# Kernel tuning notes

Measured on AMD Instinct MI355X. Metric: run time of the kernel, lower is better.

The kernel has to match this reference:

```python
import jax, jax.numpy as jnp
import numpy as np

EPS = 1e-5


def setup_inputs() -> dict:
    key = jax.random.key(0)
    ks = jax.random.split(key, 24)
    B, S, D = 32, 1024, 768        # batch, num_segs, feature_dim
    E, G, C, P = 2, 8, 64, 384     # expansion, groups, num_clusters, latent_clus_dim
    EF = E * D                     # 1536
    GFS = EF // G                  # group_feature_size = 192
    s = 0.02
    f32 = jnp.float32
    return {
        "x": jax.random.normal(ks[0], (B, S, D), f32),
        "W_exp": s * jax.random.normal(ks[1], (D, EF), f32),
        "b_exp": jnp.zeros((EF,), f32),
        "W_ga": s * jax.random.normal(ks[2], (EF, G), f32),
        "b_ga": jnp.zeros((G,), f32),
        "bn1_g": jnp.ones((G * C,), f32) + 0.1 * jax.random.normal(ks[3], (G * C,), f32),
        "bn1_b": 0.1 * jax.random.normal(ks[4], (G * C,), f32),
        "bn1_m": 0.05 * jax.random.normal(ks[5], (G * C,), f32),
        "bn1_v": 1.0 + 0.1 * jax.random.uniform(ks[6], (G * C,), f32),
        "cluster_weights": s * jax.random.normal(ks[7], (EF, G * C), f32),
        "W_proj": s * jax.random.normal(ks[8], (GFS, D), f32),
        "b_proj": jnp.zeros((D,), f32),
        "bn2_g": jnp.ones((C,), f32) + 0.1 * jax.random.normal(ks[9], (C,), f32),
        "bn2_b": 0.1 * jax.random.normal(ks[10], (C,), f32),
        "bn2_m": 0.05 * jax.random.normal(ks[11], (C,), f32),
        "bn2_v": 1.0 + 0.1 * jax.random.uniform(ks[12], (C,), f32),
        "Wq": s * jax.random.normal(ks[13], (D, P), f32),
        "bq": jnp.zeros((P,), f32),
        "Wkv": s * jax.random.normal(ks[14], (D, 2 * P), f32),
        "bkv": jnp.zeros((2 * P,), f32),
        "Wp2": s * jax.random.normal(ks[15], (P, D), f32),
        "bp2": jnp.zeros((D,), f32),
    }


def reference(x, W_exp, b_exp, W_ga, b_ga, bn1_g, bn1_b, bn1_m, bn1_v,
              cluster_weights, W_proj, b_proj, bn2_g, bn2_b, bn2_m, bn2_v,
              Wq, bq, Wkv, bkv, Wp2, bp2):
    B, S, D = x.shape
    EF = W_exp.shape[1]
    G = W_ga.shape[1]
    C = bn2_g.shape[0]
    GFS = EF // G
    P = Wq.shape[1]

    fea = x @ W_exp + b_exp                                   # (B,S,EF)
    ga = jax.nn.sigmoid(fea @ W_ga + b_ga).reshape(B, S * G)  # (B,S*G)

    act = fea.reshape(B * S, EF) @ cluster_weights            # (B*S, G*C)
    act = (act - bn1_m) * (bn1_g / jnp.sqrt(bn1_v + EPS)) + bn1_b  # eval BN
    act = jax.nn.softmax(act.reshape(B, S * G, C), axis=-1) * ga[:, :, None]

    fea_g = fea.reshape(B, S * G, GFS)
    cent = jnp.einsum('bnc,bnf->bcf', act, fea_g)             # (B,C,GFS)

    nc = cent @ W_proj + b_proj                               # (B,C,D)
    scale2 = (bn2_g / jnp.sqrt(bn2_v + EPS))[None, :, None]
    nc = (nc - bn2_m[None, :, None]) * scale2 + bn2_b[None, :, None]

    q = x @ Wq + bq                                           # (B,S,P)
    kv = (nc @ Wkv + bkv).reshape(B, C, 2, P)
    k, v = kv[:, :, 0], kv[:, :, 1]

    scores = jnp.einsum('bsp,bcp->bsc', q, k) / jnp.sqrt(jnp.float32(P))
    attn = jax.nn.softmax(scores, axis=-1)                    # (B,S,C)
    out = jnp.einsum('bsc,bcp->bsp', attn, v)                 # (B,S,P)
    return out @ Wp2 + bp2                                    # (B,S,D)
```

## Files before the change

kernel.cpp:

```cpp
#include <hip/hip_runtime.h>
#include <hip/hip_bf16.h>

#define EPSV 1e-5f

namespace {
constexpr int Bn = 32, Sn = 1024, Dn = 768, Gn = 8, Cn = 64, Pn = 384;
constexpr int EFn = 1536, GFSn = 192, Nrows = Bn * Sn;
}

typedef __attribute__((ext_vector_type(8))) short short8;
typedef __attribute__((ext_vector_type(4))) float f32x4;
typedef __attribute__((ext_vector_type(16))) float f32x16;

__device__ __forceinline__ ushort f2bf(float f) {
  uint u = __builtin_bit_cast(uint, f);
  uint r = (u + 0x7fffu + ((u >> 16) & 1u)) >> 16;
  return (ushort)r;
}
__device__ __forceinline__ uint pack2bf(float lo, float hi) {
  return (uint)f2bf(lo) | ((uint)f2bf(hi) << 16);
}
__device__ __forceinline__ float bf2f(ushort h) {
  return __builtin_bit_cast(float, (uint)h << 16);
}
__device__ __forceinline__ void load16(const ushort* g, ushort* l) {
  __builtin_amdgcn_global_load_lds(
      (const __attribute__((address_space(1))) void*)g,
      (__attribute__((address_space(3))) void*)l, 16, 0, 0);
}
__device__ __forceinline__ int xcd_lid() {
  const int nbx = gridDim.x;
  const int nwg = nbx * gridDim.y;
  const int orig = blockIdx.y * nbx + blockIdx.x;
  const int xq = nwg >> 3, xr = nwg & 7;
  const int xcd = orig & 7, xi = orig >> 3;
  return (xcd < xr ? xcd * (xq + 1) : xr * (xq + 1) + (xcd - xr) * xq) + xi;
}

template <int MODE, int TRANS>
__global__ __launch_bounds__(256) void gemm_bf16(
    const ushort* __restrict__ A, const ushort* __restrict__ BT,
    const float* __restrict__ bias, void* __restrict__ Cout,
    ushort* __restrict__ Ct, int M, int N, int K,
    const float* __restrict__ g2, const float* __restrict__ b2,
    const float* __restrict__ m2, const float* __restrict__ v2,
    ushort* __restrict__ kq, ushort* __restrict__ vt) {
  __shared__ ushort sh[16384];
  const int tid = threadIdx.x;
  const int wave = tid >> 6, lane = tid & 63;
  const int nbx = gridDim.x;
  const int lid = xcd_lid();
  const int gm = (lid / nbx) * 128, gn = (lid % nbx) * 128;
  const int wr = wave >> 1, wc = wave & 1;

  const int sws = ((tid & 3) ^ ((tid >> 3) & 3)) * 8;
  const int c0 = tid, c1 = tid + 256;
  const ushort* gA0 = A + (size_t)(gm + (c0 >> 2)) * K + sws;
  const ushort* gA1 = A + (size_t)(gm + (c1 >> 2)) * K + sws;
  const ushort* gB0 = BT + (size_t)(gn + (c0 >> 2)) * K + sws;
  const ushort* gB1 = BT + (size_t)(gn + (c1 >> 2)) * K + sws;

  f32x4 acc[4][4] = {};
  const int l15 = lane & 15;
  const int arow = wr * 64 + l15;
  const int brow = wc * 64 + l15;
  const int kswz = (((lane >> 4) ^ ((l15 >> 1) & 3))) * 8;
  const int nk = K >> 5;

#define GB_STAGE(buf, k0)                                    \
  {                                                          \
    load16(gA0 + (k0), &sh[(buf)*8192 + wave * 512]);        \
    load16(gA1 + (k0), &sh[(buf)*8192 + 2048 + wave * 512]); \
    load16(gB0 + (k0), &sh[(buf)*8192 + 4096 + wave * 512]); \
    load16(gB1 + (k0), &sh[(buf)*8192 + 6144 + wave * 512]); \
  }

  GB_STAGE(0, 0);
  for (int t = 0; t < nk; ++t) {
    const int buf = t & 1;
    if (t + 1 < nk) {
      GB_STAGE(buf ^ 1, (t + 1) * 32);
      __builtin_amdgcn_sched_barrier(0);
      asm volatile("s_waitcnt vmcnt(4)" ::: "memory");
    } else {
      asm volatile("s_waitcnt vmcnt(0)" ::: "memory");
    }
    __builtin_amdgcn_s_barrier();
    __builtin_amdgcn_sched_barrier(0);
    short8 a[4], b[4];
#pragma unroll
    for (int m = 0; m < 4; ++m)
      a[m] = *reinterpret_cast<const short8*>(
          &sh[buf * 8192 + (arow + m * 16) * 32 + kswz]);
#pragma unroll
    for (int n = 0; n < 4; ++n)
      b[n] = *reinterpret_cast<const short8*>(
          &sh[buf * 8192 + 4096 + (brow + n * 16) * 32 + kswz]);
#pragma unroll
    for (int m = 0; m < 4; ++m)
#pragma unroll
      for (int n = 0; n < 4; ++n)
        acc[m][n] = __builtin_amdgcn_mfma_f32_16x16x32_bf16(
            a[m], b[n], acc[m][n], 0, 0, 0);
    __builtin_amdgcn_s_barrier();
    __builtin_amdgcn_sched_barrier(0);
  }
#undef GB_STAGE

  const int crow0 = gm + wr * 64 + (lane >> 4) * 4;
  const int ccol0 = gn + wc * 64 + l15;
  float sc_[4][4], sf_[4][4];
  if (MODE == 2) {
#pragma unroll
    for (int m = 0; m < 4; ++m)
#pragma unroll
      for (int j = 0; j < 4; ++j) {
        const int c = (crow0 + m * 16 + j) & 63;
        const float s = g2[c] * rsqrtf(v2[c] + EPSV);
        sc_[m][j] = s;
        sf_[m][j] = b2[c] - m2[c] * s;
      }
  }
  alignas(8) ushort cb[4][4][4];
#pragma unroll
  for (int m = 0; m < 4; ++m)
#pragma unroll
    for (int n = 0; n < 4; ++n) {
      const int col = ccol0 + n * 16;
      const float bv = bias ? bias[col] : 0.f;
#pragma unroll
      for (int j = 0; j < 4; ++j) {
        const int row = crow0 + m * 16 + j;
        float v = acc[m][n][j] + bv;
        if (MODE == 0) {
          ((float*)Cout)[(size_t)row * N + col] = v;
        } else if (MODE == 1) {
          const ushort h = f2bf(v);
          ((ushort*)Cout)[(size_t)row * N + col] = h;
          if (TRANS) cb[m][n][j] = h;
        } else if (MODE == 2) {
          v = v * sc_[m][j] + sf_[m][j];
          ((ushort*)Cout)[(size_t)row * N + col] = f2bf(v);
        } else {
          const ushort h = f2bf(v);
          if (col < 384) {
            kq[(size_t)row * 384 + col] = h;
          } else {
            vt[(size_t)(row >> 6) * 24576 + (size_t)(col - 384) * 64 +
               (row & 63)] = h;
          }
        }
      }
    }

  if (TRANS) {
    const int l4 = lane >> 4;
#pragma unroll
    for (int p = 0; p < 2; ++p) {
      __syncthreads();
      if (wc == p) {
#pragma unroll
        for (int n = 0; n < 4; ++n) {
          const int cl = n * 16 + l15;
#pragma unroll
          for (int m = 0; m < 4; ++m) {
            const int r = wr * 64 + m * 16 + l4 * 4;
            *reinterpret_cast<ushort4*>(&sh[cl * 136 + r]) =
                *reinterpret_cast<const ushort4*>(&cb[m][n][0]);
          }
        }
      }
      __syncthreads();
      const int cl = tid >> 2, seg = tid & 3;
      const ushort* src = &sh[cl * 136 + seg * 32];
      ushort* dst = Ct + (size_t)(gn + p * 64 + cl) * M + gm + seg * 32;
      *reinterpret_cast<uint4*>(dst) = *reinterpret_cast<const uint4*>(src);
      *reinterpret_cast<uint4*>(dst + 8) =
          *reinterpret_cast<const uint4*>(src + 8);
      *reinterpret_cast<uint4*>(dst + 16) =
          *reinterpret_cast<const uint4*>(src + 16);
      *reinterpret_cast<uint4*>(dst + 24) =
          *reinterpret_cast<const uint4*>(src + 24);
    }
  }
}

__global__ __launch_bounds__(256) void gemm_ga(
    const ushort* __restrict__ fea, const ushort* __restrict__ WTga,
    const float* __restrict__ b_ga, float* __restrict__ ga) {
  constexpr int K = EFn;
  __shared__ ushort sh[9216];
  const int tid = threadIdx.x;
  const int wave = tid >> 6, lane = tid & 63;
  const int gm = blockIdx.x * 128;

  const int sws = ((tid & 3) ^ ((tid >> 3) & 3)) * 8;
  const int swsB = ((lane & 3) ^ ((lane >> 3) & 3)) * 8;
  const int c0 = tid, c1 = tid + 256;
  const ushort* gA0 = fea + (size_t)(gm + (c0 >> 2)) * K + sws;
  const ushort* gA1 = fea + (size_t)(gm + (c1 >> 2)) * K + sws;
  const ushort* gB = WTga + (size_t)(lane >> 2) * K + swsB;

  f32x4 acc[2] = {};
  const int l15 = lane & 15, l4 = lane >> 4;
  const int kswz = ((l4 ^ ((l15 >> 1) & 3))) * 8;

#define GA_STAGE(buf, k0)                                     \
  {                                                           \
    load16(gA0 + (k0), &sh[(buf)*4608 + wave * 512]);         \
    load16(gA1 + (k0), &sh[(buf)*4608 + 2048 + wave * 512]);  \
    if (wave == 0) load16(gB + (k0), &sh[(buf)*4608 + 4096]); \
  }

  GA_STAGE(0, 0);
  for (int t = 0; t < K / 32; ++t) {
    const int buf = t & 1;
    if (t + 1 < K / 32) {
      GA_STAGE(buf ^ 1, (t + 1) * 32);
      __builtin_amdgcn_sched_barrier(0);
      asm volatile("s_waitcnt vmcnt(2)" ::: "memory");
    } else {
      asm volatile("s_waitcnt vmcnt(0)" ::: "memory");
    }
    __builtin_amdgcn_s_barrier();
    __builtin_amdgcn_sched_barrier(0);
    const short8 b = *reinterpret_cast<const short8*>(
        &sh[buf * 4608 + 4096 + l15 * 32 + kswz]);
    short8 a[2];
#pragma unroll
    for (int mi = 0; mi < 2; ++mi)
      a[mi] = *reinterpret_cast<const short8*>(
          &sh[buf * 4608 + (wave * 32 + mi * 16 + l15) * 32 + kswz]);
#pragma unroll
    for (int mi = 0; mi < 2; ++mi)
      acc[mi] =
          __builtin_amdgcn_mfma_f32_16x16x32_bf16(a[mi], b, acc[mi], 0, 0, 0);
    __builtin_amdgcn_s_barrier();
    __builtin_amdgcn_sched_barrier(0);
  }
#undef GA_STAGE

  if (l15 < 8) {
    const float bv = b_ga[l15];
#pragma unroll
    for (int mi = 0; mi < 2; ++mi)
#pragma unroll
      for (int j = 0; j < 4; ++j) {
        const int row = gm + wave * 32 + mi * 16 + l4 * 4 + j;
        const float v = acc[mi][j] + bv;
        ga[(size_t)row * 8 + l15] = 1.0f / (1.0f + expf(-v));
      }
  }
}

__global__ __launch_bounds__(256) void gemm_sm(
    const ushort* __restrict__ A, const ushort* __restrict__ BT,
    const float* __restrict__ g1, const float* __restrict__ b1,
    const float* __restrict__ m1, const float* __restrict__ v1,
    const float* __restrict__ ga, ushort* __restrict__ actT) {
  constexpr int K = EFn, N = Nrows;
  __shared__ ushort sh[16384];
  __shared__ float sScale[128], sShift[128];
  const int tid = threadIdx.x;
  const int wave = tid >> 6, lane = tid & 63;
  const int lid = xcd_lid();
  const int gm = (lid & 3) * 128;
  const int gn = (lid >> 2) * 128;
  const int wr = wave >> 1, wc = wave & 1;

  if (tid < 128) {
    const int row = gm + tid;
    const float sc = g1[row] * rsqrtf(v1[row] + EPSV);
    sScale[tid] = sc;
    sShift[tid] = b1[row] - m1[row] * sc;
  }

  const int sws = ((tid & 3) ^ ((tid >> 3) & 3)) * 8;
  const int c0 = tid, c1 = tid + 256;
  const ushort* gA0 = A + (size_t)(gm + (c0 >> 2)) * K + sws;
  const ushort* gA1 = A + (size_t)(gm + (c1 >> 2)) * K + sws;
  const ushort* gB0 = BT + (size_t)(gn + (c0 >> 2)) * K + sws;
  const ushort* gB1 = BT + (size_t)(gn + (c1 >> 2)) * K + sws;

  f32x4 acc[4][4] = {};
  const int l15 = lane & 15;
  const int arow = wr * 64 + l15;
  const int brow = wc * 64 + l15;
  const int kswz = (((lane >> 4) ^ ((l15 >> 1) & 3))) * 8;
  const int nk = K >> 5;

#define SM_STAGE(buf, k0)                                    \
  {                                                          \
    load16(gA0 + (k0), &sh[(buf)*8192 + wave * 512]);        \
    load16(gA1 + (k0), &sh[(buf)*8192 + 2048 + wave * 512]); \
    load16(gB0 + (k0), &sh[(buf)*8192 + 4096 + wave * 512]); \
    load16(gB1 + (k0), &sh[(buf)*8192 + 6144 + wave * 512]); \
  }

  SM_STAGE(0, 0);
  for (int t = 0; t < nk; ++t) {
    const int buf = t & 1;
    if (t + 1 < nk) {
      SM_STAGE(buf ^ 1, (t + 1) * 32);
      __builtin_amdgcn_sched_barrier(0);
      asm volatile("s_waitcnt vmcnt(4)" ::: "memory");
    } else {
      asm volatile("s_waitcnt vmcnt(0)" ::: "memory");
    }
    __builtin_amdgcn_s_barrier();
    __builtin_amdgcn_sched_barrier(0);
    short8 a[4], b[4];
#pragma unroll
    for (int m = 0; m < 4; ++m)
      a[m] = *reinterpret_cast<const short8*>(
          &sh[buf * 8192 + (arow + m * 16) * 32 + kswz]);
#pragma unroll
    for (int n = 0; n < 4; ++n)
      b[n] = *reinterpret_cast<const short8*>(
          &sh[buf * 8192 + 4096 + (brow + n * 16) * 32 + kswz]);
#pragma unroll
    for (int m = 0; m < 4; ++m)
#pragma unroll
      for (int n = 0; n < 4; ++n)
        acc[m][n] = __builtin_amdgcn_mfma_f32_16x16x32_bf16(
            a[m], b[n], acc[m][n], 0, 0, 0);
    __builtin_amdgcn_s_barrier();
    __builtin_amdgcn_sched_barrier(0);
  }
#undef SM_STAGE

  const int l4 = lane >> 4;
  const int g = (gm >> 6) + wr;
#pragma unroll
  for (int n = 0; n < 4; ++n) {
    const int col = gn + wc * 64 + n * 16 + l15;
    float mx = -1e30f;
#pragma unroll
    for (int m = 0; m < 4; ++m)
#pragma unroll
      for (int j = 0; j < 4; ++j) {
        const int rl = wr * 64 + m * 16 + l4 * 4 + j;
        acc[m][n][j] = acc[m][n][j] * sScale[rl] + sShift[rl];
        mx = fmaxf(mx, acc[m][n][j]);
      }
    mx = fmaxf(mx, __shfl_xor(mx, 16));
    mx = fmaxf(mx, __shfl_xor(mx, 32));
    float sum = 0.f;
#pragma unroll
    for (int m = 0; m < 4; ++m)
#pragma unroll
      for (int j = 0; j < 4; ++j) {
        acc[m][n][j] = expf(acc[m][n][j] - mx);
        sum += acc[m][n][j];
      }
    sum += __shfl_xor(sum, 16);
    sum += __shfl_xor(sum, 32);
    const float sc = ga[(size_t)col * 8 + g] / sum;
#pragma unroll
    for (int m = 0; m < 4; ++m)
#pragma unroll
      for (int j = 0; j < 4; ++j) {
        const int rowg = gm + wr * 64 + m * 16 + l4 * 4 + j;
        actT[(size_t)rowg * N + col] = f2bf(acc[m][n][j] * sc);
      }
  }
}

__global__ __launch_bounds__(256) void cvt_kernel(const float* __restrict__ in,
                                                  ushort* __restrict__ out,
                                                  int n4) {
  const int i = blockIdx.x * 256 + threadIdx.x;
  if (i >= n4) return;
  const float4 v = reinterpret_cast<const float4*>(in)[i];
  ushort4 o;
  o.x = f2bf(v.x); o.y = f2bf(v.y); o.z = f2bf(v.z); o.w = f2bf(v.w);
  reinterpret_cast<ushort4*>(out)[i] = o;
}

__global__ __launch_bounds__(256) void tconv_kernel(const float* __restrict__ in,
                                                    ushort* __restrict__ out,
                                                    int R, int C) {
  __shared__ float t[32][33];
  const int tx = threadIdx.x & 31, ty = threadIdx.x >> 5;
  const int bc = blockIdx.x * 32, br = blockIdx.y * 32;
#pragma unroll
  for (int i = 0; i < 32; i += 8)
    t[ty + i][tx] = in[(size_t)(br + ty + i) * C + bc + tx];
  __syncthreads();
#pragma unroll
  for (int i = 0; i < 32; i += 8)
    out[(size_t)(bc + ty + i) * R + br + tx] = f2bf(t[tx][ty + i]);
}

__global__ __launch_bounds__(256) void gawt_kernel(const float* __restrict__ in,
                                                   ushort* __restrict__ out) {
  const int k = blockIdx.x * 256 + threadIdx.x;
#pragma unroll
  for (int g = 0; g < 8; ++g) {
    out[(size_t)g * EFn + k] = f2bf(in[(size_t)k * 8 + g]);
    out[(size_t)(g + 8) * EFn + k] = 0;
  }
}

__global__ __launch_bounds__(256) void cent_mfma(
    const ushort* __restrict__ actT, const ushort* __restrict__ feaT,
    float* __restrict__ part) {
  __shared__ ushort As[2][64 * 64];
  __shared__ ushort Bs[2][192 * 64];
  const int tid = threadIdx.x;
  const int wave = tid >> 6, lane = tid & 63;
  const int b = blockIdx.x >> 4;
  const int g = (blockIdx.x >> 1) & 7;
  const int ch = blockIdx.x & 1;
  const size_t colbase = (size_t)b * 1024 + ch * 512;
  const int srow = tid >> 2, scp = (tid & 3) * 2;
  const ushort* gA = actT + (size_t)(g * 64 + srow) * Nrows + colbase;
  const ushort* gB0 = feaT + (size_t)(g * 192 + srow) * Nrows + colbase;
  const ushort* gB1 = gB0 + (size_t)64 * Nrows;
  const ushort* gB2 = gB0 + (size_t)128 * Nrows;

  uint4 ra[2], rb0[2], rb1[2], rb2[2];
  f32x4 acc[4][3] = {};
  const int l15 = lane & 15, hi = lane >> 4;
  const int sw = srow & 7;

#define CM_ISSUE(k0)                                                    \
  {                                                                     \
    _Pragma("unroll") for (int i = 0; i < 2; ++i) {                     \
      const int off = (k0) + (scp + i) * 8;                             \
      ra[i] = *reinterpret_cast<const uint4*>(gA + off);                \
      rb0[i] = *reinterpret_cast<const uint4*>(gB0 + off);              \
      rb1[i] = *reinterpret_cast<const uint4*>(gB1 + off);              \
      rb2[i] = *reinterpret_cast<const uint4*>(gB2 + off);              \
    }                                                                   \
  }
#define CM_STASH(buf)                                                   \
  {                                                                     \
    _Pragma("unroll") for (int i = 0; i < 2; ++i) {                     \
      const int c = scp + i;                                            \
      *reinterpret_cast<uint4*>(&As[buf][srow * 64 + ((c ^ sw) * 8)]) = \
          ra[i];                                                        \
      *reinterpret_cast<uint4*>(&Bs[buf][srow * 64 + ((c ^ sw) * 8)]) = \
          rb0[i];                                                       \
      *reinterpret_cast<uint4*>(                                        \
          &Bs[buf][(64 + srow) * 64 + ((c ^ sw) * 8)]) = rb1[i];        \
      *reinterpret_cast<uint4*>(                                        \
          &Bs[buf][(128 + srow) * 64 + ((c ^ sw) * 8)]) = rb2[i];       \
    }                                                                   \
  }

  CM_ISSUE(0);
  CM_STASH(0);
  for (int kk = 0; kk < 8; ++kk) {
    const int buf = kk & 1;
    __syncthreads();
    if (kk < 7) CM_ISSUE((kk + 1) * 64);
#pragma unroll
    for (int ks = 0; ks < 2; ++ks) {
      const int chh = ks * 4 + hi;
      short8 a[4], bb[3];
#pragma unroll
      for (int m = 0; m < 4; ++m) {
        const int r = m * 16 + l15;
        a[m] = *reinterpret_cast<const short8*>(
            &As[buf][r * 64 + ((chh ^ (r & 7)) * 8)]);
      }
#pragma unroll
      for (int nn = 0; nn < 3; ++nn) {
        const int r = wave * 48 + nn * 16 + l15;
        bb[nn] = *reinterpret_cast<const short8*>(
            &Bs[buf][r * 64 + ((chh ^ (r & 7)) * 8)]);
      }
#pragma unroll
      for (int m = 0; m < 4; ++m)
#pragma unroll
        for (int nn = 0; nn < 3; ++nn)
          acc[m][nn] = __builtin_amdgcn_mfma_f32_16x16x32_bf16(
              a[m], bb[nn], acc[m][nn], 0, 0, 0);
    }
    if (kk < 7) CM_STASH(buf ^ 1);
  }
#undef CM_ISSUE
#undef CM_STASH

  float* pb = part + (size_t)blockIdx.x * 12288;
#pragma unroll
  for (int m = 0; m < 4; ++m)
#pragma unroll
    for (int nn = 0; nn < 3; ++nn) {
      const int col = wave * 48 + nn * 16 + l15;
#pragma unroll
      for (int j = 0; j < 4; ++j) {
        const int row = m * 16 + hi * 4 + j;
        pb[row * 192 + col] = acc[m][nn][j];
      }
    }
}

__global__ __launch_bounds__(256) void cent_reduce8(
    const float* __restrict__ part, ushort* __restrict__ cent) {
  const int idx = blockIdx.x * 256 + threadIdx.x;
  const int b = idx / 12288, r = idx % 12288;
  float s = 0.f;
#pragma unroll
  for (int j = 0; j < 16; ++j) s += part[(size_t)(b * 16 + j) * 12288 + r];
  cent[idx] = f2bf(s);
}

__global__ __launch_bounds__(256) void attn_mfma(
    const ushort* __restrict__ qb, const ushort* __restrict__ kb,
    const ushort* __restrict__ vtb, ushort* __restrict__ aout) {
  const int wave = threadIdx.x >> 6, lane = threadIdx.x & 63;
  const int wrow = blockIdx.x * 4 + wave;
  const int row0 = wrow * 32;
  const int b = row0 >> 10;
  const int l31 = lane & 31, hi = lane >> 5;

  f32x16 accs0 = 0.f, accs1 = 0.f;
  const ushort* qp = qb + (size_t)(row0 + l31) * 384 + hi * 8;
  const ushort* kp = kb + (size_t)(b * 64 + l31) * 384 + hi * 8;
#pragma unroll 4
  for (int ks = 0; ks < 24; ++ks) {
    const short8 bq = *reinterpret_cast<const short8*>(qp + ks * 16);
    const short8 a0 = *reinterpret_cast<const short8*>(kp + ks * 16);
    const short8 a1 = *reinterpret_cast<const short8*>(kp + 32 * 384 + ks * 16);
    accs0 = __builtin_amdgcn_mfma_f32_32x32x16_bf16(a0, bq, accs0, 0, 0, 0);
    accs1 = __builtin_amdgcn_mfma_f32_32x32x16_bf16(a1, bq, accs1, 0, 0, 0);
  }

  const float alpha = 0.05103103630798287f;
  float p[32];
#pragma unroll
  for (int i = 0; i < 16; ++i) { p[i] = accs0[i]; p[16 + i] = accs1[i]; }
  float mx = p[0];
#pragma unroll
  for (int i = 1; i < 32; ++i) mx = fmaxf(mx, p[i]);
  mx = fmaxf(mx, __shfl_xor(mx, 32));
  float sum = 0.f;
#pragma unroll
  for (int i = 0; i < 32; ++i) {
    p[i] = expf((p[i] - mx) * alpha);
    sum += p[i];
  }
  sum += __shfl_xor(sum, 32);
  const float inv = 1.0f / sum;

  uint pk0[8], pk1[8];
#pragma unroll
  for (int ct = 0; ct < 2; ++ct)
#pragma unroll
    for (int rg = 0; rg < 4; ++rg) {
      pk0[ct * 4 + rg] =
          pack2bf(p[ct * 16 + rg * 4 + 0] * inv, p[ct * 16 + rg * 4 + 1] * inv);
      pk1[ct * 4 + rg] =
          pack2bf(p[ct * 16 + rg * 4 + 2] * inv, p[ct * 16 + rg * 4 + 3] * inv);
    }
  uint ex0[8], ex1[8];
#pragma unroll
  for (int i = 0; i < 8; ++i) {
    ex0[i] = __shfl_xor(pk0[i], 32);
    ex1[i] = __shfl_xor(pk1[i], 32);
  }

  const ushort* vp = vtb + ((size_t)b * 384 + l31) * 64 + hi * 8;
  ushort* orow = aout + (size_t)(row0 + l31) * 384;
  for (int mt = 0; mt < 12; ++mt) {
    f32x16 acco = 0.f;
#pragma unroll
    for (int kc = 0; kc < 4; ++kc) {
      const short8 av = *reinterpret_cast<const short8*>(
          vp + (size_t)mt * 32 * 64 + kc * 16);
      const int base = (kc >> 1) * 4 + (kc & 1) * 2;
      const uint o0 = hi ? pk0[base + 1] : pk0[base];
      const uint o1 = hi ? pk1[base + 1] : pk1[base];
      const uint e0 = hi ? ex0[base + 1] : ex0[base];
      const uint e1 = hi ? ex1[base + 1] : ex1[base];
      uint4 uu;
      uu.x = hi ? e0 : o0;
      uu.y = hi ? e1 : o1;
      uu.z = hi ? o0 : e0;
      uu.w = hi ? o1 : e1;
      const short8 bp = __builtin_bit_cast(short8, uu);
      acco = __builtin_amdgcn_mfma_f32_32x32x16_bf16(av, bp, acco, 0, 0, 0);
    }
#pragma unroll
    for (int rg = 0; rg < 4; ++rg) {
      ushort4 ov;
      ov.x = f2bf(acco[rg * 4 + 0]);
      ov.y = f2bf(acco[rg * 4 + 1]);
      ov.z = f2bf(acco[rg * 4 + 2]);
      ov.w = f2bf(acco[rg * 4 + 3]);
      *reinterpret_cast<ushort4*>(&orow[mt * 32 + rg * 8 + hi * 4]) = ov;
    }
  }
}

extern "C" void kernel_launch(void* const* d_in, const int* in_sizes, int n_in,
                              void* d_out, int out_size, void* d_ws,
                              size_t ws_size, hipStream_t stream) {
  (void)in_sizes; (void)n_in; (void)out_size; (void)ws_size;
  const float* x      = (const float*)d_in[0];
  const float* W_exp  = (const float*)d_in[1];
  const float* b_exp  = (const float*)d_in[2];
  const float* W_ga   = (const float*)d_in[3];
  const float* b_ga   = (const float*)d_in[4];
  const float* bn1_g  = (const float*)d_in[5];
  const float* bn1_b  = (const float*)d_in[6];
  const float* bn1_m  = (const float*)d_in[7];
  const float* bn1_v  = (const float*)d_in[8];
  const float* cw     = (const float*)d_in[9];
  const float* W_proj = (const float*)d_in[10];
  const float* b_proj = (const float*)d_in[11];
  const float* bn2_g  = (const float*)d_in[12];
  const float* bn2_b  = (const float*)d_in[13];
  const float* bn2_m  = (const float*)d_in[14];
  const float* bn2_v  = (const float*)d_in[15];
  const float* Wq     = (const float*)d_in[16];
  const float* bq     = (const float*)d_in[17];
  const float* Wkv    = (const float*)d_in[18];
  const float* bkv    = (const float*)d_in[19];
  const float* Wp2    = (const float*)d_in[20];
  const float* bp2    = (const float*)d_in[21];
  float* out = (float*)d_out;

  char* ws = (char*)d_ws;
  ushort* fea  = (ushort*)(ws + 0);
  ushort* aout = (ushort*)(ws + 0);
  ushort* xb   = (ushort*)(ws + 100663296ull);
  ushort* actT = (ushort*)(ws + 100663296ull);
  ushort* q_bf = (ushort*)(ws + 150994944ull);
  float*  ga   = (float*)(ws + 176160768ull);
  float*  part = (float*)(ws + 177209344ull);
  ushort* WT1  = (ushort*)(ws + 202375168ull);
  ushort* WT2  = (ushort*)(ws + 204734464ull);
  ushort* WT3  = (ushort*)(ws + 206307328ull);
  ushort* WT4  = (ushort*)(ws + 206897152ull);
  ushort* WT5  = (ushort*)(ws + 207486976ull);
  ushort* WT6  = (ushort*)(ws + 207781888ull);
  ushort* WTga = (ushort*)(ws + 208961536ull);
  ushort* cent = (ushort*)(ws + 209010688ull);
  ushort* nc   = (ushort*)(ws + 209797120ull);
  ushort* k_bf = (ushort*)(ws + 212942848ull);
  ushort* vT_bf= (ushort*)(ws + 214515712ull);
  ushort* feaT = (ushort*)d_out;

  dim3 blk(256);
  cvt_kernel<<<dim3((Nrows * Dn / 4 + 255) / 256), blk, 0, stream>>>(
      x, xb, Nrows * Dn / 4);
  tconv_kernel<<<dim3(EFn / 32, Dn / 32), blk, 0, stream>>>(W_exp, WT1, Dn, EFn);
  tconv_kernel<<<dim3(512 / 32, EFn / 32), blk, 0, stream>>>(cw, WT2, EFn, 512);
  tconv_kernel<<<dim3(Pn / 32, Dn / 32), blk, 0, stream>>>(Wq, WT3, Dn, Pn);
  tconv_kernel<<<dim3(Dn / 32, Pn / 32), blk, 0, stream>>>(Wp2, WT4, Pn, Dn);
  tconv_kernel<<<dim3(Dn / 32, GFSn / 32), blk, 0, stream>>>(W_proj, WT5, GFSn, Dn);
  tconv_kernel<<<dim3(Dn / 32, Dn / 32), blk, 0, stream>>>(Wkv, WT6, Dn, Dn);
  gawt_kernel<<<dim3(EFn / 256), blk, 0, stream>>>(W_ga, WTga);
  gemm_bf16<1, 1><<<dim3(EFn / 128, Nrows / 128), blk, 0, stream>>>(
      xb, WT1, b_exp, fea, feaT, Nrows, EFn, Dn,
      nullptr, nullptr, nullptr, nullptr, nullptr, nullptr);
  gemm_bf16<1, 0><<<dim3(Pn / 128, Nrows / 128), blk, 0, stream>>>(
      xb, WT3, bq, q_bf, nullptr, Nrows, Pn, Dn,
      nullptr, nullptr, nullptr, nullptr, nullptr, nullptr);
  gemm_ga<<<dim3(Nrows / 128), blk, 0, stream>>>(fea, WTga, b_ga, ga);
  gemm_sm<<<dim3(Nrows / 128, 512 / 128), blk, 0, stream>>>(
      WT2, fea, bn1_g, bn1_b, bn1_m, bn1_v, ga, actT);
  cent_mfma<<<dim3(Bn * Gn * 2), blk, 0, stream>>>(actT, feaT, part);
  cent_reduce8<<<dim3(393216 / 256), blk, 0, stream>>>(part, cent);
  gemm_bf16<2, 0><<<dim3(Dn / 128, 2048 / 128), blk, 0, stream>>>(
      cent, WT5, b_proj, nc, nullptr, 2048, Dn, GFSn,
      bn2_g, bn2_b, bn2_m, bn2_v, nullptr, nullptr);
  gemm_bf16<3, 0><<<dim3(Dn / 128, 2048 / 128), blk, 0, stream>>>(
      nc, WT6, bkv, nullptr, nullptr, 2048, Dn, Dn,
      nullptr, nullptr, nullptr, nullptr, k_bf, vT_bf);
  attn_mfma<<<dim3(Nrows / 128), blk, 0, stream>>>(q_bf, k_bf, vT_bf, aout);
  gemm_bf16<0, 0><<<dim3(Dn / 128, Nrows / 128), blk, 0, stream>>>(
      aout, WT4, bp2, out, nullptr, Nrows, Dn, Pn,
      nullptr, nullptr, nullptr, nullptr, nullptr, nullptr);
}
```

Baseline: 465.4 us.

## Triple-buffer GEMM pipelines and drop transposed fea copy in centroid kernel

Moves gemm_bf16, gemm_ga and gemm_sm from double to triple buffered LDS staging, prefetching two K-tiles ahead with adjusted waitcnts to hide more global latency. Also removes the transposed feaT output written by the expansion GEMM. cent_mfma now reads the row-major fea directly and transposes it in registers before storing to LDS. This cuts a large transposed global write and its LDS shuffle, at the cost of strided loads in cent_mfma and more LDS per block, which may lower occupancy.

```diff
diff --git a/kernel.cpp b/kernel.cpp
--- a/kernel.cpp
+++ b/kernel.cpp
@@ -37,15 +37,15 @@
   return (xcd < xr ? xcd * (xq + 1) : xr * (xq + 1) + (xcd - xr) * xq) + xi;
 }
 
-template <int MODE, int TRANS>
+template <int MODE>
 __global__ __launch_bounds__(256) void gemm_bf16(
     const ushort* __restrict__ A, const ushort* __restrict__ BT,
     const float* __restrict__ bias, void* __restrict__ Cout,
-    ushort* __restrict__ Ct, int M, int N, int K,
+    int M, int N, int K,
     const float* __restrict__ g2, const float* __restrict__ b2,
     const float* __restrict__ m2, const float* __restrict__ v2,
     ushort* __restrict__ kq, ushort* __restrict__ vt) {
-  __shared__ ushort sh[16384];
+  __shared__ ushort sh[24576];
   const int tid = threadIdx.x;
   const int wave = tid >> 6, lane = tid & 63;
   const int nbx = gridDim.x;
@@ -76,11 +76,15 @@
   }
 
   GB_STAGE(0, 0);
+  GB_STAGE(1, 32);
+  int bc = 0;
   for (int t = 0; t < nk; ++t) {
-    const int buf = t & 1;
-    if (t + 1 < nk) {
-      GB_STAGE(buf ^ 1, (t + 1) * 32);
+    if (t + 2 < nk) {
+      const int bp = (bc == 0) ? 2 : bc - 1;
+      GB_STAGE(bp, (t + 2) * 32);
       __builtin_amdgcn_sched_barrier(0);
+      asm volatile("s_waitcnt vmcnt(8)" ::: "memory");
+    } else if (t + 1 < nk) {
       asm volatile("s_waitcnt vmcnt(4)" ::: "memory");
     } else {
       asm volatile("s_waitcnt vmcnt(0)" ::: "memory");
@@ -91,11 +95,11 @@
 #pragma unroll
     for (int m = 0; m < 4; ++m)
       a[m] = *reinterpret_cast<const short8*>(
-          &sh[buf * 8192 + (arow + m * 16) * 32 + kswz]);
+          &sh[bc * 8192 + (arow + m * 16) * 32 + kswz]);
 #pragma unroll
     for (int n = 0; n < 4; ++n)
       b[n] = *reinterpret_cast<const short8*>(
-          &sh[buf * 8192 + 4096 + (brow + n * 16) * 32 + kswz]);
+          &sh[bc * 8192 + 4096 + (brow + n * 16) * 32 + kswz]);
 #pragma unroll
     for (int m = 0; m < 4; ++m)
 #pragma unroll
@@ -104,6 +108,7 @@
             a[m], b[n], acc[m][n], 0, 0, 0);
     __builtin_amdgcn_s_barrier();
     __builtin_amdgcn_sched_barrier(0);
+    bc = (bc == 2) ? 0 : bc + 1;
   }
 #undef GB_STAGE
 
@@ -121,7 +126,6 @@
         sf_[m][j] = b2[c] - m2[c] * s;
       }
   }
-  alignas(8) ushort cb[4][4][4];
 #pragma unroll
   for (int m = 0; m < 4; ++m)
 #pragma unroll
@@ -135,9 +139,7 @@
         if (MODE == 0) {
           ((float*)Cout)[(size_t)row * N + col] = v;
         } else if (MODE == 1) {
-          const ushort h = f2bf(v);
-          ((ushort*)Cout)[(size_t)row * N + col] = h;
-          if (TRANS) cb[m][n][j] = h;
+          ((ushort*)Cout)[(size_t)row * N + col] = f2bf(v);
         } else if (MODE == 2) {
           v = v * sc_[m][j] + sf_[m][j];
           ((ushort*)Cout)[(size_t)row * N + col] = f2bf(v);
@@ -152,44 +154,13 @@
         }
       }
     }
-
-  if (TRANS) {
-    const int l4 = lane >> 4;
-#pragma unroll
-    for (int p = 0; p < 2; ++p) {
-      __syncthreads();
-      if (wc == p) {
-#pragma unroll
-        for (int n = 0; n < 4; ++n) {
-          const int cl = n * 16 + l15;
-#pragma unroll
-          for (int m = 0; m < 4; ++m) {
-            const int r = wr * 64 + m * 16 + l4 * 4;
-            *reinterpret_cast<ushort4*>(&sh[cl * 136 + r]) =
-                *reinterpret_cast<const ushort4*>(&cb[m][n][0]);
-          }
-        }
-      }
-      __syncthreads();
-      const int cl = tid >> 2, seg = tid & 3;
-      const ushort* src = &sh[cl * 136 + seg * 32];
-      ushort* dst = Ct + (size_t)(gn + p * 64 + cl) * M + gm + seg * 32;
-      *reinterpret_cast<uint4*>(dst) = *reinterpret_cast<const uint4*>(src);
-      *reinterpret_cast<uint4*>(dst + 8) =
-          *reinterpret_cast<const uint4*>(src + 8);
-      *reinterpret_cast<uint4*>(dst + 16) =
-          *reinterpret_cast<const uint4*>(src + 16);
-      *reinterpret_cast<uint4*>(dst + 24) =
-          *reinterpret_cast<const uint4*>(src + 24);
-    }
-  }
 }
 
 __global__ __launch_bounds__(256) void gemm_ga(
     const ushort* __restrict__ fea, const ushort* __restrict__ WTga,
     const float* __restrict__ b_ga, float* __restrict__ ga) {
   constexpr int K = EFn;
-  __shared__ ushort sh[9216];
+  __shared__ ushort sh[13824];
   const int tid = threadIdx.x;
   const int wave = tid >> 6, lane = tid & 63;
   const int gm = blockIdx.x * 128;
@@ -204,6 +175,7 @@
   f32x4 acc[2] = {};
   const int l15 = lane & 15, l4 = lane >> 4;
   const int kswz = ((l4 ^ ((l15 >> 1) & 3))) * 8;
+  constexpr int nk = K / 32;
 
 #define GA_STAGE(buf, k0)                                     \
   {                                                           \
@@ -213,30 +185,41 @@
   }
 
   GA_STAGE(0, 0);
-  for (int t = 0; t < K / 32; ++t) {
-    const int buf = t & 1;
-    if (t + 1 < K / 32) {
-      GA_STAGE(buf ^ 1, (t + 1) * 32);
+  GA_STAGE(1, 32);
+  int bc = 0;
+  for (int t = 0; t < nk; ++t) {
+    if (t + 2 < nk) {
+      const int bp = (bc == 0) ? 2 : bc - 1;
+      GA_STAGE(bp, (t + 2) * 32);
       __builtin_amdgcn_sched_barrier(0);
-      asm volatile("s_waitcnt vmcnt(2)" ::: "memory");
+      if (wave == 0)
+        asm volatile("s_waitcnt vmcnt(6)" ::: "memory");
+      else
+        asm volatile("s_waitcnt vmcnt(4)" ::: "memory");
+    } else if (t + 1 < nk) {
+      if (wave == 0)
+        asm volatile("s_waitcnt vmcnt(3)" ::: "memory");
+      else
+        asm volatile("s_waitcnt vmcnt(2)" ::: "memory");
     } else {
       asm volatile("s_waitcnt vmcnt(0)" ::: "memory");
     }
     __builtin_amdgcn_s_barrier();
     __builtin_amdgcn_sched_barrier(0);
     const short8 b = *reinterpret_cast<const short8*>(
-        &sh[buf * 4608 + 4096 + l15 * 32 + kswz]);
+        &sh[bc * 4608 + 4096 + l15 * 32 + kswz]);
     short8 a[2];
 #pragma unroll
     for (int mi = 0; mi < 2; ++mi)
       a[mi] = *reinterpret_cast<const short8*>(
-          &sh[buf * 4608 + (wave * 32 + mi * 16 + l15) * 32 + kswz]);
+          &sh[bc * 4608 + (wave * 32 + mi * 16 + l15) * 32 + kswz]);
 #pragma unroll
     for (int mi = 0; mi < 2; ++mi)
       acc[mi] =
           __builtin_amdgcn_mfma_f32_16x16x32_bf16(a[mi], b, acc[mi], 0, 0, 0);
     __builtin_amdgcn_s_barrier();
     __builtin_amdgcn_sched_barrier(0);
+    bc = (bc == 2) ? 0 : bc + 1;
   }
 #undef GA_STAGE
 
@@ -259,7 +242,7 @@
     const float* __restrict__ m1, const float* __restrict__ v1,
     const float* __restrict__ ga, ushort* __restrict__ actT) {
   constexpr int K = EFn, N = Nrows;
-  __shared__ ushort sh[16384];
+  __shared__ ushort sh[24576];
   __shared__ float sScale[128], sShift[128];
   const int tid = threadIdx.x;
   const int wave = tid >> 6, lane = tid & 63;
@@ -287,7 +270,7 @@
   const int arow = wr * 64 + l15;
   const int brow = wc * 64 + l15;
   const int kswz = (((lane >> 4) ^ ((l15 >> 1) & 3))) * 8;
-  const int nk = K >> 5;
+  constexpr int nk = K >> 5;
 
 #define SM_STAGE(buf, k0)                                    \
   {                                                          \
@@ -298,11 +281,15 @@
   }
 
   SM_STAGE(0, 0);
+  SM_STAGE(1, 32);
+  int bc = 0;
   for (int t = 0; t < nk; ++t) {
-    const int buf = t & 1;
-    if (t + 1 < nk) {
-      SM_STAGE(buf ^ 1, (t + 1) * 32);
+    if (t + 2 < nk) {
+      const int bp = (bc == 0) ? 2 : bc - 1;
+      SM_STAGE(bp, (t + 2) * 32);
       __builtin_amdgcn_sched_barrier(0);
+      asm volatile("s_waitcnt vmcnt(8)" ::: "memory");
+    } else if (t + 1 < nk) {
       asm volatile("s_waitcnt vmcnt(4)" ::: "memory");
     } else {
       asm volatile("s_waitcnt vmcnt(0)" ::: "memory");
@@ -313,11 +300,11 @@
 #pragma unroll
     for (int m = 0; m < 4; ++m)
       a[m] = *reinterpret_cast<const short8*>(
-          &sh[buf * 8192 + (arow + m * 16) * 32 + kswz]);
+          &sh[bc * 8192 + (arow + m * 16) * 32 + kswz]);
 #pragma unroll
     for (int n = 0; n < 4; ++n)
       b[n] = *reinterpret_cast<const short8*>(
-          &sh[buf * 8192 + 4096 + (brow + n * 16) * 32 + kswz]);
+          &sh[bc * 8192 + 4096 + (brow + n * 16) * 32 + kswz]);
 #pragma unroll
     for (int m = 0; m < 4; ++m)
 #pragma unroll
@@ -326,6 +313,7 @@
             a[m], b[n], acc[m][n], 0, 0, 0);
     __builtin_amdgcn_s_barrier();
     __builtin_amdgcn_sched_barrier(0);
+    bc = (bc == 2) ? 0 : bc + 1;
   }
 #undef SM_STAGE
 
@@ -403,7 +391,7 @@
 }
 
 __global__ __launch_bounds__(256) void cent_mfma(
-    const ushort* __restrict__ actT, const ushort* __restrict__ feaT,
+    const ushort* __restrict__ actT, const ushort* __restrict__ fea,
     float* __restrict__ part) {
   __shared__ ushort As[2][64 * 64];
   __shared__ ushort Bs[2][192 * 64];
@@ -415,38 +403,44 @@
   const size_t colbase = (size_t)b * 1024 + ch * 512;
   const int srow = tid >> 2, scp = (tid & 3) * 2;
   const ushort* gA = actT + (size_t)(g * 64 + srow) * Nrows + colbase;
-  const ushort* gB0 = feaT + (size_t)(g * 192 + srow) * Nrows + colbase;
-  const ushort* gB1 = gB0 + (size_t)64 * Nrows;
-  const ushort* gB2 = gB0 + (size_t)128 * Nrows;
-
-  uint4 ra[2], rb0[2], rb1[2], rb2[2];
+  const int bseg = tid % 24;
+  const int bsg = tid / 24;
+  const bool bact = tid < 192;
+  const ushort* gB =
+      fea + (size_t)(colbase + bsg * 8) * EFn + g * 192 + bseg * 8;
+
+  uint4 ra[2], rbv[8];
   f32x4 acc[4][3] = {};
   const int l15 = lane & 15, hi = lane >> 4;
   const int sw = srow & 7;
 
-#define CM_ISSUE(k0)                                                    \
-  {                                                                     \
-    _Pragma("unroll") for (int i = 0; i < 2; ++i) {                     \
-      const int off = (k0) + (scp + i) * 8;                             \
-      ra[i] = *reinterpret_cast<const uint4*>(gA + off);                \
-      rb0[i] = *reinterpret_cast<const uint4*>(gB0 + off);              \
-      rb1[i] = *reinterpret_cast<const uint4*>(gB1 + off);              \
-      rb2[i] = *reinterpret_cast<const uint4*>(gB2 + off);              \
-    }                                                                   \
-  }
-#define CM_STASH(buf)                                                   \
-  {                                                                     \
-    _Pragma("unroll") for (int i = 0; i < 2; ++i) {                     \
-      const int c = scp + i;                                            \
-      *reinterpret_cast<uint4*>(&As[buf][srow * 64 + ((c ^ sw) * 8)]) = \
-          ra[i];                                                        \
-      *reinterpret_cast<uint4*>(&Bs[buf][srow * 64 + ((c ^ sw) * 8)]) = \
-          rb0[i];                                                       \
-      *reinterpret_cast<uint4*>(                                        \
-          &Bs[buf][(64 + srow) * 64 + ((c ^ sw) * 8)]) = rb1[i];        \
-      *reinterpret_cast<uint4*>(                                        \
-          &Bs[buf][(128 + srow) * 64 + ((c ^ sw) * 8)]) = rb2[i];       \
-    }                                                                   \
+#define CM_ISSUE(k0)                                                        \
+  {                                                                         \
+    _Pragma("unroll") for (int i = 0; i < 2; ++i) ra[i] =                   \
+        *reinterpret_cast<const uint4*>(gA + (k0) + (scp + i) * 8);         \
+    if (bact) {                                                             \
+      _Pragma("unroll") for (int i = 0; i < 8; ++i) rbv[i] =                \
+          *reinterpret_cast<const uint4*>(gB + (size_t)((k0) + i) * EFn);   \
+    }                                                                       \
+  }
+#define CM_STASH(buf)                                                       \
+  {                                                                         \
+    _Pragma("unroll") for (int i = 0; i < 2; ++i) {                         \
+      const int c = scp + i;                                                \
+      *reinterpret_cast<uint4*>(&As[buf][srow * 64 + ((c ^ sw) * 8)]) =     \
+          ra[i];                                                            \
+    }                                                                       \
+    if (bact) {                                                             \
+      const ushort* rin = reinterpret_cast<const ushort*>(rbv);             \
+      _Pragma("unroll") for (int e = 0; e < 8; ++e) {                       \
+        alignas(16) ushort tmp[8];                                          \
+        _Pragma("unroll") for (int i = 0; i < 8; ++i) tmp[i] =              \
+            rin[i * 8 + e];                                                 \
+        const int r = bseg * 8 + e;                                         \
+        *reinterpret_cast<uint4*>(&Bs[buf][r * 64 + ((bsg ^ (r & 7)) * 8)]) \
+            = *reinterpret_cast<const uint4*>(tmp);                         \
+      }                                                                     \
+    }                                                                       \
   }
 
   CM_ISSUE(0);
@@ -642,7 +636,6 @@
   ushort* nc   = (ushort*)(ws + 209797120ull);
   ushort* k_bf = (ushort*)(ws + 212942848ull);
   ushort* vT_bf= (ushort*)(ws + 214515712ull);
-  ushort* feaT = (ushort*)d_out;
 
   dim3 blk(256);
   cvt_kernel<<<dim3((Nrows * Dn / 4 + 255) / 256), blk, 0, stream>>>(
@@ -654,25 +647,25 @@
   tconv_kernel<<<dim3(Dn / 32, GFSn / 32), blk, 0, stream>>>(W_proj, WT5, GFSn, Dn);
   tconv_kernel<<<dim3(Dn / 32, Dn / 32), blk, 0, stream>>>(Wkv, WT6, Dn, Dn);
   gawt_kernel<<<dim3(EFn / 256), blk, 0, stream>>>(W_ga, WTga);
-  gemm_bf16<1, 1><<<dim3(EFn / 128, Nrows / 128), blk, 0, stream>>>(
-      xb, WT1, b_exp, fea, feaT, Nrows, EFn, Dn,
+  gemm_bf16<1><<<dim3(EFn / 128, Nrows / 128), blk, 0, stream>>>(
+      xb, WT1, b_exp, fea, Nrows, EFn, Dn,
       nullptr, nullptr, nullptr, nullptr, nullptr, nullptr);
-  gemm_bf16<1, 0><<<dim3(Pn / 128, Nrows / 128), blk, 0, stream>>>(
-      xb, WT3, bq, q_bf, nullptr, Nrows, Pn, Dn,
+  gemm_bf16<1><<<dim3(Pn / 128, Nrows / 128), blk, 0, stream>>>(
+      xb, WT3, bq, q_bf, Nrows, Pn, Dn,
       nullptr, nullptr, nullptr, nullptr, nullptr, nullptr);
   gemm_ga<<<dim3(Nrows / 128), blk, 0, stream>>>(fea, WTga, b_ga, ga);
   gemm_sm<<<dim3(Nrows / 128, 512 / 128), blk, 0, stream>>>(
       WT2, fea, bn1_g, bn1_b, bn1_m, bn1_v, ga, actT);
-  cent_mfma<<<dim3(Bn * Gn * 2), blk, 0, stream>>>(actT, feaT, part);
+  cent_mfma<<<dim3(Bn * Gn * 2), blk, 0, stream>>>(actT, fea, part);
   cent_reduce8<<<dim3(393216 / 256), blk, 0, stream>>>(part, cent);
-  gemm_bf16<2, 0><<<dim3(Dn / 128, 2048 / 128), blk, 0, stream>>>(
-      cent, WT5, b_proj, nc, nullptr, 2048, Dn, GFSn,
+  gemm_bf16<2><<<dim3(Dn / 128, 2048 / 128), blk, 0, stream>>>(
+      cent, WT5, b_proj, nc, 2048, Dn, GFSn,
       bn2_g, bn2_b, bn2_m, bn2_v, nullptr, nullptr);
-  gemm_bf16<3, 0><<<dim3(Dn / 128, 2048 / 128), blk, 0, stream>>>(
-      nc, WT6, bkv, nullptr, nullptr, 2048, Dn, Dn,
+  gemm_bf16<3><<<dim3(Dn / 128, 2048 / 128), blk, 0, stream>>>(
+      nc, WT6, bkv, nullptr, 2048, Dn, Dn,
       nullptr, nullptr, nullptr, nullptr, k_bf, vT_bf);
   attn_mfma<<<dim3(Nrows / 128), blk, 0, stream>>>(q_bf, k_bf, vT_bf, aout);
-  gemm_bf16<0, 0><<<dim3(Dn / 128, Nrows / 128), blk, 0, stream>>>(
-      aout, WT4, bp2, out, nullptr, Nrows, Dn, Pn,
+  gemm_bf16<0><<<dim3(Dn / 128, Nrows / 128), blk, 0, stream>>>(
+      aout, WT4, bp2, out, Nrows, Dn, Pn,
       nullptr, nullptr, nullptr, nullptr, nullptr, nullptr);
 }
```

Result: faster. 405.0 us (median of 2 runs) (-13.0%).
